# Kernel tuning notes

Hardware: AMD Instinct MI355X
Metric: run time of the kernel (lower is better)

Reference implementation:

```python
import jax, jax.numpy as jnp
import numpy as np

B, N, E, F = 4, 4096, 65536, 128


def setup_inputs() -> dict:
    key = jax.random.key(0)
    ks = jax.random.split(key, 16)
    s = 0.02
    inp = {
        'node_feats': jax.random.normal(ks[0], (B, N, F), jnp.float32),
        'edge_feats': jax.random.normal(ks[1], (B, E, F), jnp.float32),
        'i': jax.random.randint(ks[2], (E,), 0, N, jnp.int32),
        'j': jax.random.randint(ks[3], (E,), 0, N, jnp.int32),
        'W_src_gate': jax.random.normal(ks[4], (F, F), jnp.float32) * s,
        'b_src_gate': jnp.zeros((F,), jnp.float32),
        'W_dst_gate': jax.random.normal(ks[5], (F, F), jnp.float32) * s,
        'b_dst_gate': jnp.zeros((F,), jnp.float32),
        'W_edge_gate': jax.random.normal(ks[6], (F, F), jnp.float32) * s,
        'b_edge_gate': jnp.zeros((F,), jnp.float32),
        'W_src_update': jax.random.normal(ks[7], (F, F), jnp.float32) * s,
        'b_src_update': jnp.zeros((F,), jnp.float32),
        'W_dst_update': jax.random.normal(ks[8], (F, F), jnp.float32) * s,
        'b_dst_update': jnp.zeros((F,), jnp.float32),
    }
    return inp


def _linear(x, W, b):
    # torch nn.Linear: x @ W.T + b, W is [out, in]
    return jnp.einsum('bnf,gf->bng', x, W) + b


def reference(node_feats, edge_feats, i, j,
              W_src_gate, b_src_gate, W_dst_gate, b_dst_gate,
              W_edge_gate, b_edge_gate, W_src_update, b_src_update,
              W_dst_update, b_dst_update):
    Bn, Nn, Fn = node_feats.shape
    e_src = _linear(node_feats, W_src_gate, b_src_gate)[:, i]      # [B, E, F]
    e_dst = _linear(node_feats, W_dst_gate, b_dst_gate)[:, j]      # [B, E, F]
    y = e_src + e_dst + _linear(edge_feats, W_edge_gate, b_edge_gate)
    sigma = jax.nn.sigmoid(y)
    bh = _linear(node_feats, W_dst_update, b_dst_update)[:, j]     # [B, E, F]
    m = bh * sigma
    # scatter-add over edges into destination nodes (along dim 1)
    zeros = jnp.zeros((Bn, Nn, Fn), node_feats.dtype)
    sum_sigma_h = zeros.at[:, i].add(m)
    sum_sigma = zeros.at[:, i].add(sigma)
    h = sum_sigma_h / (sum_sigma + 1e-6)
    x = jax.nn.silu(_linear(node_feats, W_src_update, b_src_update) + h)
    y = jax.nn.silu(y)
    # residual=True
    x = node_feats + x
    y = edge_feats + y
    return (x, y)
```

## Files before the change

kernel.cpp:

```cpp
#include <hip/hip_runtime.h>
#include <hip/hip_bf16.h>

typedef __attribute__((ext_vector_type(8))) short short8;
typedef __attribute__((ext_vector_type(4))) float f32x4;
typedef __attribute__((ext_vector_type(2))) float f32x2;

#define DEVI __device__ __forceinline__

static constexpr int NB = 4;
static constexpr int NN = 4096;
static constexpr int NE = 65536;
static constexpr int MROWS = NB * NN;
static constexpr int TILES = 4;

DEVI short f2b(float f) {
    __hip_bfloat16 h = __float2bfloat16(f);
    return *reinterpret_cast<short*>(&h);
}
DEVI float b2f(ushort u) {
    uint v = (uint)u << 16;
    float f;
    __builtin_memcpy(&f, &v, 4);
    return f;
}

__global__ void prep_weights(const float* __restrict__ w0, const float* __restrict__ w1,
                             const float* __restrict__ w2, const float* __restrict__ w3,
                             const float* __restrict__ w4, ushort* __restrict__ out) {
    int idx = blockIdx.x * 256 + threadIdx.x;
    int wsel = idx >> 14;
    int off = idx & 16383;
    const float* src = wsel == 0 ? w0 : wsel == 1 ? w1 : wsel == 2 ? w2 : wsel == 3 ? w3 : w4;
    out[idx] = (ushort)f2b(src[off]);
}

__global__ void hist_kernel(const int* __restrict__ iIdx, int* __restrict__ cnt) {
    int e = blockIdx.x * 256 + threadIdx.x;
    atomicAdd(&cnt[iIdx[e]], 1);
}

__global__ __launch_bounds__(256) void scan_kernel(const int* __restrict__ cnt,
                                                   int* __restrict__ start) {
    __shared__ int ls[256];
    int t = threadIdx.x;
    int base = t * 16;
    int loc[16];
    int s = 0;
#pragma unroll
    for (int q = 0; q < 16; ++q) { loc[q] = s; s += cnt[base + q]; }
    ls[t] = s;
    __syncthreads();
    for (int off = 1; off < 256; off <<= 1) {
        int v = (t >= off) ? ls[t - off] : 0;
        __syncthreads();
        ls[t] += v;
        __syncthreads();
    }
    int ex = ls[t] - s;
#pragma unroll
    for (int q = 0; q < 16; ++q) start[base + q] = ex + loc[q];
    if (t == 255) start[4096] = ex + s;
}

__global__ void scatter_kernel(const int* __restrict__ iIdx, const int* __restrict__ jIdx,
                               const int* __restrict__ start, int* __restrict__ cur,
                               int* __restrict__ rank, int* __restrict__ jsort) {
    int e = blockIdx.x * 256 + threadIdx.x;
    int iv = iIdx[e];
    int pos = start[iv] + atomicAdd(&cur[iv], 1);
    rank[e] = pos;
    jsort[pos] = jIdx[e];
}

DEVI void stage_W(const ushort* __restrict__ Wg, ushort* Wl, int tid) {
    int n = tid >> 1;
    int kh = (tid & 1) * 64;
#pragma unroll
    for (int c = 0; c < 8; ++c) {
        int k = kh + c * 8;
        short8 v = *reinterpret_cast<const short8*>(Wg + n * 128 + k);
        int byt = (n * 256 + k * 2) ^ ((n & 7) << 4);
        *reinterpret_cast<short8*>(reinterpret_cast<char*>(Wl) + byt) = v;
    }
}

DEVI void load_afrag(const float* __restrict__ rowptr, int kgrp, short8 afrag[4]) {
#pragma unroll
    for (int ks = 0; ks < 4; ++ks) {
        int k0 = ks * 32 + kgrp * 8;
        f32x4 lo = *reinterpret_cast<const f32x4*>(rowptr + k0);
        f32x4 hi = *reinterpret_cast<const f32x4*>(rowptr + k0 + 4);
        short8 a;
#pragma unroll
        for (int q = 0; q < 4; ++q) a[q] = f2b(lo[q]);
#pragma unroll
        for (int q = 0; q < 4; ++q) a[4 + q] = f2b(hi[q]);
        afrag[ks] = a;
    }
}

DEVI void mfma_frags(const short8 afrag[4], const ushort* __restrict__ Wl,
                     int lane, f32x4 acc[8]) {
    const int colb = lane & 15;
    const int kgrp = lane >> 4;
#pragma unroll
    for (int nt = 0; nt < 8; ++nt) acc[nt] = f32x4{0.f, 0.f, 0.f, 0.f};
#pragma unroll
    for (int ks = 0; ks < 4; ++ks) {
#pragma unroll
        for (int nt = 0; nt < 8; ++nt) {
            int n = nt * 16 + colb;
            int byt = (n * 256 + (ks * 32 + kgrp * 8) * 2) ^ ((n & 7) << 4);
            short8 bfrag = *reinterpret_cast<const short8*>(
                reinterpret_cast<const char*>(Wl) + byt);
            acc[nt] = __builtin_amdgcn_mfma_f32_16x16x32_bf16(afrag[ks], bfrag, acc[nt], 0, 0, 0);
        }
    }
}

__global__ __launch_bounds__(256) void node_proj_kernel(
    const float* __restrict__ node_feats,
    const ushort* __restrict__ Wbf,
    const float* __restrict__ bias0, const float* __restrict__ bias1,
    const float* __restrict__ bias2, const float* __restrict__ bias3,
    ushort* __restrict__ P)
{
    __shared__ ushort Wl[128 * 128];
    const int widx = blockIdx.y;
    const int row0 = blockIdx.x * 64;
    const int tid = threadIdx.x;

    stage_W(Wbf + (size_t)widx * 16384, Wl, tid);
    __syncthreads();

    const int lane = tid & 63, wv = tid >> 6;
    const int colb = lane & 15, kgrp = lane >> 4;
    short8 afrag[4];
    load_afrag(node_feats + (size_t)(row0 + wv * 16 + colb) * 128, kgrp, afrag);
    f32x4 acc[8];
    mfma_frags(afrag, Wl, lane, acc);

    const float* bias = widx == 0 ? bias0 : widx == 1 ? bias1 : widx == 2 ? bias2 : bias3;
    ushort* Po = P + (size_t)widx * MROWS * 128;
#pragma unroll
    for (int r = 0; r < 4; ++r) {
        int row = row0 + wv * 16 + kgrp * 4 + r;
#pragma unroll
        for (int nt = 0; nt < 8; ++nt) {
            int col = nt * 16 + colb;
            Po[(size_t)row * 128 + col] = (ushort)f2b(acc[nt][r] + bias[col]);
        }
    }
}

__global__ __launch_bounds__(256) void edge_kernel(
    const float* __restrict__ edge_feats,
    const int* __restrict__ iIdx, const int* __restrict__ jIdx,
    const int* __restrict__ rank,
    const ushort* __restrict__ Weg,
    const float* __restrict__ b_eg,
    const ushort* __restrict__ Psg, const ushort* __restrict__ Pdg,
    ushort* __restrict__ sigS,
    float* __restrict__ yOut)
{
    __shared__ ushort Wl[128 * 128];
    const int b = blockIdx.y;
    const int tid = threadIdx.x;

    stage_W(Weg, Wl, tid);
    __syncthreads();

    const int lane = tid & 63, wv = tid >> 6;
    const int colb = lane & 15, kgrp = lane >> 4;
    const float* Ab = edge_feats + (size_t)b * NE * 128;
    const size_t nbase = (size_t)b * NN;

    float bg[8];
#pragma unroll
    for (int nt = 0; nt < 8; ++nt) bg[nt] = b_eg[nt * 16 + colb];

    for (int t = 0; t < TILES; ++t) {
        const int e0 = (blockIdx.x * TILES + t) * 64;
        short8 afrag[4];
        load_afrag(Ab + (size_t)(e0 + wv * 16 + colb) * 128, kgrp, afrag);
        f32x4 acc[8];
        mfma_frags(afrag, Wl, lane, acc);

#pragma unroll
        for (int r = 0; r < 4; ++r) {
            int erow = wv * 16 + kgrp * 4 + r;
            int e = e0 + erow;
            int ie = iIdx[e], je = jIdx[e], rk = rank[e];
            const ushort* sg = Psg + (nbase + ie) * 128;
            const ushort* dg = Pdg + (nbase + je) * 128;
            const float* ef = Ab + (size_t)e * 128;
            float* yo = yOut + ((size_t)b * NE + e) * 128;
            ushort* so = sigS + ((size_t)b * NE + rk) * 128;
#pragma unroll
            for (int nt = 0; nt < 8; ++nt) {
                int col = nt * 16 + colb;
                float y = acc[nt][r] + bg[nt] + b2f(sg[col]) + b2f(dg[col]);
                float sig = 1.0f / (1.0f + __expf(-y));
                yo[col] = ef[col] + y * sig;
                so[col] = (ushort)f2b(sig);
            }
        }
    }
}

__global__ __launch_bounds__(256) void node_reduce_kernel(
    const ushort* __restrict__ sigS,
    const int* __restrict__ start,
    const int* __restrict__ jsort,
    const ushort* __restrict__ Pdu,
    const ushort* __restrict__ Psu,
    const float* __restrict__ nf,
    float* __restrict__ xOut)
{
    int task = blockIdx.x * 4 + (threadIdx.x >> 6);
    int lane = threadIdx.x & 63;
    int b = task >> 12;
    int n = task & 4095;
    int s0 = start[n], s1 = start[n + 1];

    const size_t ebase = (size_t)b * NE;
    const size_t nbase = (size_t)b * NN;

    float S0 = 0.f, S1 = 0.f, Sh0 = 0.f, Sh1 = 0.f;
    for (int k = s0; k < s1; ++k) {
        int j = jsort[k];
        uint sg2 = *reinterpret_cast<const uint*>(sigS + (ebase + k) * 128 + lane * 2);
        uint du2 = *reinterpret_cast<const uint*>(Pdu + (nbase + j) * 128 + lane * 2);
        float sa = b2f((ushort)(sg2 & 0xffff));
        float sb = b2f((ushort)(sg2 >> 16));
        float da = b2f((ushort)(du2 & 0xffff));
        float db = b2f((ushort)(du2 >> 16));
        S0 += sa; S1 += sb;
        Sh0 += da * sa; Sh1 += db * sb;
    }

    size_t off = (nbase + n) * 128 + lane * 2;
    uint su2 = *reinterpret_cast<const uint*>(Psu + off);
    f32x2 a = *reinterpret_cast<const f32x2*>(nf + off);
    float h0 = Sh0 / (S0 + 1e-6f);
    float h1 = Sh1 / (S1 + 1e-6f);
    float v0 = b2f((ushort)(su2 & 0xffff)) + h0;
    float v1 = b2f((ushort)(su2 >> 16)) + h1;
    f32x2 r;
    r[0] = a[0] + v0 / (1.f + __expf(-v0));
    r[1] = a[1] + v1 / (1.f + __expf(-v1));
    *reinterpret_cast<f32x2*>(xOut + off) = r;
}

extern "C" void kernel_launch(void* const* d_in, const int* in_sizes, int n_in,
                              void* d_out, int out_size, void* d_ws, size_t ws_size,
                              hipStream_t stream) {
    (void)in_sizes; (void)n_in; (void)out_size; (void)ws_size;

    const float* node_feats = (const float*)d_in[0];
    const float* edge_feats = (const float*)d_in[1];
    const int* iIdx = (const int*)d_in[2];
    const int* jIdx = (const int*)d_in[3];
    const float* Wsg = (const float*)d_in[4];  const float* bsg = (const float*)d_in[5];
    const float* Wdg = (const float*)d_in[6];  const float* bdg = (const float*)d_in[7];
    const float* Weg = (const float*)d_in[8];  const float* beg = (const float*)d_in[9];
    const float* Wsu = (const float*)d_in[10]; const float* bsu = (const float*)d_in[11];
    const float* Wdu = (const float*)d_in[12]; const float* bdu = (const float*)d_in[13];

    float* out = (float*)d_out;
    float* xOut = out;
    float* yOut = out + (size_t)MROWS * 128;

    ushort* sigS = (ushort*)d_ws;
    ushort* P = sigS + (size_t)NB * NE * 128;
    ushort* Wbf = P + (size_t)4 * MROWS * 128;
    int* rank = (int*)(Wbf + 5 * 16384);
    int* jsort = rank + NE;
    int* cnt = jsort + NE;
    int* cur = cnt + 4096;
    int* start = cur + 4096;

    hipMemsetAsync(cnt, 0, 2 * 4096 * sizeof(int), stream);

    prep_weights<<<(5 * 16384) / 256, 256, 0, stream>>>(Wsg, Wdg, Wdu, Wsu, Weg, Wbf);

    hist_kernel<<<NE / 256, 256, 0, stream>>>(iIdx, cnt);
    scan_kernel<<<1, 256, 0, stream>>>(cnt, start);
    scatter_kernel<<<NE / 256, 256, 0, stream>>>(iIdx, jIdx, start, cur, rank, jsort);

    dim3 gA(MROWS / 64, 4);
    node_proj_kernel<<<gA, 256, 0, stream>>>(node_feats, Wbf, bsg, bdg, bdu, bsu, P);

    dim3 gB(NE / (64 * TILES), NB);
    edge_kernel<<<gB, 256, 0, stream>>>(edge_feats, iIdx, jIdx, rank,
                                        Wbf + (size_t)4 * 16384, beg,
                                        P,
                                        P + (size_t)1 * MROWS * 128,
                                        sigS, yOut);

    node_reduce_kernel<<<MROWS / 4, 256, 0, stream>>>(
        sigS, start, jsort,
        P + (size_t)2 * MROWS * 128,
        P + (size_t)3 * MROWS * 128,
        node_feats, xOut);
}
```

Measured before the change: 191.3 us.

## Read bf16 weights straight from global memory, drop LDS staging, and unroll the reduce loop

The GEMM kernels stop staging the 128x128 bf16 weight matrix into shared memory and read MFMA B-fragments directly from global (L1/L2-cached) memory. node_proj now computes all four projections per block from a single A-fragment load instead of launching one block per weight. The edge kernel processes one 64-row tile per block instead of four, and launch bounds request higher occupancy. The reduce loop is unrolled by four so several gather loads are in flight at once. The tradeoff is more global/L2 traffic for weights and uncoalesced 16-byte B-fragment reads in exchange for removing LDS staging, barriers and LDS capacity limits on occupancy.

```diff
diff --git a/kernel.cpp b/kernel.cpp
--- a/kernel.cpp
+++ b/kernel.cpp
@@ -11,7 +11,6 @@
 static constexpr int NN = 4096;
 static constexpr int NE = 65536;
 static constexpr int MROWS = NB * NN;
-static constexpr int TILES = 4;
 
 DEVI short f2b(float f) {
     __hip_bfloat16 h = __float2bfloat16(f);
@@ -72,18 +71,6 @@
     jsort[pos] = jIdx[e];
 }
 
-DEVI void stage_W(const ushort* __restrict__ Wg, ushort* Wl, int tid) {
-    int n = tid >> 1;
-    int kh = (tid & 1) * 64;
-#pragma unroll
-    for (int c = 0; c < 8; ++c) {
-        int k = kh + c * 8;
-        short8 v = *reinterpret_cast<const short8*>(Wg + n * 128 + k);
-        int byt = (n * 256 + k * 2) ^ ((n & 7) << 4);
-        *reinterpret_cast<short8*>(reinterpret_cast<char*>(Wl) + byt) = v;
-    }
-}
-
 DEVI void load_afrag(const float* __restrict__ rowptr, int kgrp, short8 afrag[4]) {
 #pragma unroll
     for (int ks = 0; ks < 4; ++ks) {
@@ -99,8 +86,8 @@
     }
 }
 
-DEVI void mfma_frags(const short8 afrag[4], const ushort* __restrict__ Wl,
-                     int lane, f32x4 acc[8]) {
+DEVI void mfma_frags_g(const short8 afrag[4], const ushort* __restrict__ Wg,
+                       int lane, f32x4 acc[8]) {
     const int colb = lane & 15;
     const int kgrp = lane >> 4;
 #pragma unroll
@@ -109,51 +96,48 @@
     for (int ks = 0; ks < 4; ++ks) {
 #pragma unroll
         for (int nt = 0; nt < 8; ++nt) {
-            int n = nt * 16 + colb;
-            int byt = (n * 256 + (ks * 32 + kgrp * 8) * 2) ^ ((n & 7) << 4);
-            short8 bfrag = *reinterpret_cast<const short8*>(
-                reinterpret_cast<const char*>(Wl) + byt);
+            const short8 bfrag = *reinterpret_cast<const short8*>(
+                Wg + (nt * 16 + colb) * 128 + ks * 32 + kgrp * 8);
             acc[nt] = __builtin_amdgcn_mfma_f32_16x16x32_bf16(afrag[ks], bfrag, acc[nt], 0, 0, 0);
         }
     }
 }
 
-__global__ __launch_bounds__(256) void node_proj_kernel(
+__global__ __launch_bounds__(256, 8) void node_proj_kernel(
     const float* __restrict__ node_feats,
     const ushort* __restrict__ Wbf,
     const float* __restrict__ bias0, const float* __restrict__ bias1,
     const float* __restrict__ bias2, const float* __restrict__ bias3,
     ushort* __restrict__ P)
 {
-    __shared__ ushort Wl[128 * 128];
-    const int widx = blockIdx.y;
     const int row0 = blockIdx.x * 64;
     const int tid = threadIdx.x;
-
-    stage_W(Wbf + (size_t)widx * 16384, Wl, tid);
-    __syncthreads();
-
     const int lane = tid & 63, wv = tid >> 6;
     const int colb = lane & 15, kgrp = lane >> 4;
+
     short8 afrag[4];
     load_afrag(node_feats + (size_t)(row0 + wv * 16 + colb) * 128, kgrp, afrag);
-    f32x4 acc[8];
-    mfma_frags(afrag, Wl, lane, acc);
-
-    const float* bias = widx == 0 ? bias0 : widx == 1 ? bias1 : widx == 2 ? bias2 : bias3;
-    ushort* Po = P + (size_t)widx * MROWS * 128;
-#pragma unroll
-    for (int r = 0; r < 4; ++r) {
-        int row = row0 + wv * 16 + kgrp * 4 + r;
-#pragma unroll
-        for (int nt = 0; nt < 8; ++nt) {
-            int col = nt * 16 + colb;
-            Po[(size_t)row * 128 + col] = (ushort)f2b(acc[nt][r] + bias[col]);
-        }
-    }
-}
-
-__global__ __launch_bounds__(256) void edge_kernel(
+
+    const float* biases[4] = {bias0, bias1, bias2, bias3};
+#pragma unroll
+    for (int w = 0; w < 4; ++w) {
+        f32x4 acc[8];
+        mfma_frags_g(afrag, Wbf + (size_t)w * 16384, lane, acc);
+        const float* bias = biases[w];
+        ushort* Po = P + (size_t)w * MROWS * 128;
+#pragma unroll
+        for (int r = 0; r < 4; ++r) {
+            int row = row0 + wv * 16 + kgrp * 4 + r;
+#pragma unroll
+            for (int nt = 0; nt < 8; ++nt) {
+                int col = nt * 16 + colb;
+                Po[(size_t)row * 128 + col] = (ushort)f2b(acc[nt][r] + bias[col]);
+            }
+        }
+    }
+}
+
+__global__ __launch_bounds__(256, 8) void edge_kernel(
     const float* __restrict__ edge_feats,
     const int* __restrict__ iIdx, const int* __restrict__ jIdx,
     const int* __restrict__ rank,
@@ -163,52 +147,41 @@
     ushort* __restrict__ sigS,
     float* __restrict__ yOut)
 {
-    __shared__ ushort Wl[128 * 128];
     const int b = blockIdx.y;
+    const int e0 = blockIdx.x * 64;
     const int tid = threadIdx.x;
-
-    stage_W(Weg, Wl, tid);
-    __syncthreads();
-
     const int lane = tid & 63, wv = tid >> 6;
     const int colb = lane & 15, kgrp = lane >> 4;
     const float* Ab = edge_feats + (size_t)b * NE * 128;
     const size_t nbase = (size_t)b * NN;
 
-    float bg[8];
-#pragma unroll
-    for (int nt = 0; nt < 8; ++nt) bg[nt] = b_eg[nt * 16 + colb];
-
-    for (int t = 0; t < TILES; ++t) {
-        const int e0 = (blockIdx.x * TILES + t) * 64;
-        short8 afrag[4];
-        load_afrag(Ab + (size_t)(e0 + wv * 16 + colb) * 128, kgrp, afrag);
-        f32x4 acc[8];
-        mfma_frags(afrag, Wl, lane, acc);
-
-#pragma unroll
-        for (int r = 0; r < 4; ++r) {
-            int erow = wv * 16 + kgrp * 4 + r;
-            int e = e0 + erow;
-            int ie = iIdx[e], je = jIdx[e], rk = rank[e];
-            const ushort* sg = Psg + (nbase + ie) * 128;
-            const ushort* dg = Pdg + (nbase + je) * 128;
-            const float* ef = Ab + (size_t)e * 128;
-            float* yo = yOut + ((size_t)b * NE + e) * 128;
-            ushort* so = sigS + ((size_t)b * NE + rk) * 128;
-#pragma unroll
-            for (int nt = 0; nt < 8; ++nt) {
-                int col = nt * 16 + colb;
-                float y = acc[nt][r] + bg[nt] + b2f(sg[col]) + b2f(dg[col]);
-                float sig = 1.0f / (1.0f + __expf(-y));
-                yo[col] = ef[col] + y * sig;
-                so[col] = (ushort)f2b(sig);
-            }
-        }
-    }
-}
-
-__global__ __launch_bounds__(256) void node_reduce_kernel(
+    short8 afrag[4];
+    load_afrag(Ab + (size_t)(e0 + wv * 16 + colb) * 128, kgrp, afrag);
+    f32x4 acc[8];
+    mfma_frags_g(afrag, Weg, lane, acc);
+
+#pragma unroll
+    for (int r = 0; r < 4; ++r) {
+        int erow = wv * 16 + kgrp * 4 + r;
+        int e = e0 + erow;
+        int ie = iIdx[e], je = jIdx[e], rk = rank[e];
+        const ushort* sg = Psg + (nbase + ie) * 128;
+        const ushort* dg = Pdg + (nbase + je) * 128;
+        const float* ef = Ab + (size_t)(e0 + erow) * 128;
+        float* yo = yOut + ((size_t)b * NE + e) * 128;
+        ushort* so = sigS + ((size_t)b * NE + rk) * 128;
+#pragma unroll
+        for (int nt = 0; nt < 8; ++nt) {
+            int col = nt * 16 + colb;
+            float y = acc[nt][r] + b_eg[col] + b2f(sg[col]) + b2f(dg[col]);
+            float sig = 1.0f / (1.0f + __expf(-y));
+            yo[col] = ef[col] + y * sig;
+            so[col] = (ushort)f2b(sig);
+        }
+    }
+}
+
+__global__ __launch_bounds__(256, 8) void node_reduce_kernel(
     const ushort* __restrict__ sigS,
     const int* __restrict__ start,
     const int* __restrict__ jsort,
@@ -227,14 +200,29 @@
     const size_t nbase = (size_t)b * NN;
 
     float S0 = 0.f, S1 = 0.f, Sh0 = 0.f, Sh1 = 0.f;
-    for (int k = s0; k < s1; ++k) {
+    int k = s0;
+    for (; k + 4 <= s1; k += 4) {
+        uint sv[4], dv[4];
+#pragma unroll
+        for (int q = 0; q < 4; ++q) {
+            int j = jsort[k + q];
+            sv[q] = *reinterpret_cast<const uint*>(sigS + (ebase + k + q) * 128 + lane * 2);
+            dv[q] = *reinterpret_cast<const uint*>(Pdu + (nbase + j) * 128 + lane * 2);
+        }
+#pragma unroll
+        for (int q = 0; q < 4; ++q) {
+            float sa = b2f((ushort)(sv[q] & 0xffff)), sb = b2f((ushort)(sv[q] >> 16));
+            float da = b2f((ushort)(dv[q] & 0xffff)), db = b2f((ushort)(dv[q] >> 16));
+            S0 += sa; S1 += sb;
+            Sh0 += da * sa; Sh1 += db * sb;
+        }
+    }
+    for (; k < s1; ++k) {
         int j = jsort[k];
         uint sg2 = *reinterpret_cast<const uint*>(sigS + (ebase + k) * 128 + lane * 2);
         uint du2 = *reinterpret_cast<const uint*>(Pdu + (nbase + j) * 128 + lane * 2);
-        float sa = b2f((ushort)(sg2 & 0xffff));
-        float sb = b2f((ushort)(sg2 >> 16));
-        float da = b2f((ushort)(du2 & 0xffff));
-        float db = b2f((ushort)(du2 >> 16));
+        float sa = b2f((ushort)(sg2 & 0xffff)), sb = b2f((ushort)(sg2 >> 16));
+        float da = b2f((ushort)(du2 & 0xffff)), db = b2f((ushort)(du2 >> 16));
         S0 += sa; S1 += sb;
         Sh0 += da * sa; Sh1 += db * sb;
     }
@@ -288,10 +276,9 @@
     scan_kernel<<<1, 256, 0, stream>>>(cnt, start);
     scatter_kernel<<<NE / 256, 256, 0, stream>>>(iIdx, jIdx, start, cur, rank, jsort);
 
-    dim3 gA(MROWS / 64, 4);
-    node_proj_kernel<<<gA, 256, 0, stream>>>(node_feats, Wbf, bsg, bdg, bdu, bsu, P);
-
-    dim3 gB(NE / (64 * TILES), NB);
+    node_proj_kernel<<<MROWS / 64, 256, 0, stream>>>(node_feats, Wbf, bsg, bdg, bdu, bsu, P);
+
+    dim3 gB(NE / 64, NB);
     edge_kernel<<<gB, 256, 0, stream>>>(edge_feats, iIdx, jIdx, rank,
                                         Wbf + (size_t)4 * 16384, beg,
                                         P,
```

Measured after the change: 311.1 us. 1.63x slower.
